# Performance work log

Hardware: AMD Instinct MI355X
Metric: run time of the kernel (lower is better)

Reference implementation:

```python
import jax, jax.numpy as jnp
import numpy as np

B, T, D, E, H, K = 4, 4096, 1024, 8, 512, 2  # batch, seq, n_embed, num_experts, bottleneck, top_k


def setup_inputs() -> dict:
    key = jax.random.key(0)
    ks = jax.random.split(key, 8)
    s = 0.02  # param scale (original zero-inits adapters; random used for a meaningful baseline)
    return {
        "x": jax.random.normal(ks[0], (B, T, D), jnp.float32),
        "Wr": (jax.random.normal(ks[1], (D, E), jnp.float32) * s),
        "br": jnp.zeros((E,), jnp.float32),
        "Wn": (jax.random.normal(ks[2], (D, E), jnp.float32) * s),
        "bn": jnp.zeros((E,), jnp.float32),
        "Wd": (jax.random.normal(ks[3], (E, D, H), jnp.float32) * s),
        "bd": jnp.zeros((E, H), jnp.float32),
        "Wu": (jax.random.normal(ks[4], (E, H, D), jnp.float32) * s),
        "bu": jnp.zeros((E, D), jnp.float32),
        "noise": jax.random.normal(ks[5], (B, T, E), jnp.float32),
        "top_k": K,
    }


def reference(x, Wr, br, Wn, bn, Wd, bd, Wu, bu, noise, top_k):
    # --- NoisyTopkRouter ---
    logits = x @ Wr + br                                   # [B,T,E]
    noise_logits = x @ Wn + bn                             # [B,T,E]
    noisy = logits + noise * jax.nn.softplus(noise_logits)  # randn * softplus(noise_logits)
    _, idx = jax.lax.top_k(noisy, top_k)                   # [B,T,K]
    # mask of selected experts; where(mask, noisy, -inf) == scatter(top_k_logits into -inf)
    mask = jax.nn.one_hot(idx, noisy.shape[-1], dtype=jnp.bool_).any(axis=-2)  # [B,T,E]
    sparse = jnp.where(mask, noisy, -jnp.inf)
    gates = jax.nn.softmax(sparse, axis=-1)                # zeros for unselected experts

    # --- Experts (dense grouped form; gate==0 exactly kills unselected experts incl. biases) ---
    down = jnp.einsum('btd,edh->bteh', x, Wd) + bd         # [B,T,E,H]
    hidden = jax.nn.gelu(down, approximate=False)          # torch GELU is exact (erf)
    up = jnp.einsum('bteh,ehd->bted', hidden, Wu) + bu     # [B,T,E,D]
    return jnp.einsum('bted,bte->btd', up, gates)          # gate-weighted combine
```

## Files before the change

kernel.cpp:

```cpp
#include <hip/hip_runtime.h>
#include <hip/hip_bf16.h>
#include <hip/hip_fp16.h>
#include <math.h>

#define DD   1024
#define EE   8
#define HH   512
#define NTOK 16384
#define NG   16
#define MAXMT 24

typedef __attribute__((ext_vector_type(8))) short short8;
typedef __attribute__((ext_vector_type(4))) float floatx4;

__device__ __forceinline__ ushort f2bfu(float f) {
    __hip_bfloat16 h = __float2bfloat16(f);
    return *reinterpret_cast<ushort*>(&h);
}
__device__ __forceinline__ float bfu2f(ushort u) {
    union { unsigned u; float f; } cv; cv.u = ((unsigned)u) << 16; return cv.f;
}

__device__ __forceinline__ void glds16(const void* g, void* l) {
    __builtin_amdgcn_global_load_lds(
        (const __attribute__((address_space(1))) unsigned int*)g,
        (__attribute__((address_space(3))) unsigned int*)l, 16, 0, 0);
}

__global__ __launch_bounds__(256) void trans_k(const float* __restrict__ src, ushort* __restrict__ dst,
                                               const int R, const int C, int* __restrict__ cnt) {
    if (cnt && blockIdx.x == 0 && blockIdx.y == 0 && blockIdx.z == 0 && threadIdx.x < 256)
        cnt[threadIdx.x] = 0;
    const int e = blockIdx.z, r0 = blockIdx.y * 64, c0 = blockIdx.x * 64;
    __shared__ float t[64][65];
    const int tid = threadIdx.x;
    const int cseg = (tid & 15) * 4, rr = tid >> 4;
#pragma unroll
    for (int j = 0; j < 4; ++j) {
        const int r = rr + j * 16;
        const float4 v = *(const float4*)(src + ((size_t)e * R + r0 + r) * C + c0 + cseg);
        t[r][cseg] = v.x; t[r][cseg+1] = v.y; t[r][cseg+2] = v.z; t[r][cseg+3] = v.w;
    }
    __syncthreads();
    const int rseg = (tid & 15) * 4;
#pragma unroll
    for (int j = 0; j < 4; ++j) {
        const int crow = (tid >> 4) + j * 16;
        ushort o[4];
#pragma unroll
        for (int q = 0; q < 4; ++q) o[q] = f2bfu(t[rseg + q][crow]);
        *(uint2*)(dst + ((size_t)e * C + c0 + crow) * R + r0 + rseg) = *(uint2*)o;
    }
}

#define ROUTER_TAIL(AR, AN, T) do {                                           \
    const int t_ = (T);                                                       \
    float noisy[EE];                                                          \
    _Pragma("unroll")                                                         \
    for (int e = 0; e < EE; ++e) {                                            \
        const float lg = AR[e] + br[e];                                       \
        const float nl = AN[e] + bn[e];                                       \
        const float sp = fmaxf(nl, 0.f) + log1pf(expf(-fabsf(nl)));           \
        noisy[e] = lg + noise[(size_t)t_ * EE + e] * sp;                      \
    }                                                                         \
    int i0 = 0;                                                               \
    _Pragma("unroll")                                                         \
    for (int e = 1; e < EE; ++e) if (noisy[e] > noisy[i0]) i0 = e;            \
    int i1 = (i0 == 0) ? 1 : 0;                                               \
    _Pragma("unroll")                                                         \
    for (int e = 0; e < EE; ++e) if (e != i0 && noisy[e] > noisy[i1]) i1 = e; \
    const float ex = expf(noisy[i1] - noisy[i0]);                             \
    const float g0 = 1.f / (1.f + ex);                                        \
    const float g1 = ex / (1.f + ex);                                         \
    __half h0 = __float2half_rn(g0), h1 = __float2half_rn(g1);                \
    const unsigned u0 = (unsigned)t_ | ((unsigned)*reinterpret_cast<ushort*>(&h0) << 16); \
    const unsigned u1 = (unsigned)t_ | ((unsigned)*reinterpret_cast<ushort*>(&h1) << 16); \
    const int ga = i0 * 2 + 0, gb = i1 * 2 + 1;                               \
    int p0 = atomicAdd(&cnt[ga * 16], 1);                                     \
    entries[ga * NTOK + p0] = u0;                                             \
    int p1 = atomicAdd(&cnt[gb * 16], 1);                                     \
    entries[gb * NTOK + p1] = u1;                                             \
} while (0)

__global__ __launch_bounds__(512) void router_k(
    const float* __restrict__ x, const float* __restrict__ Wr, const float* __restrict__ br,
    const float* __restrict__ Wn, const float* __restrict__ bn, const float* __restrict__ noise,
    int* __restrict__ cnt, unsigned* __restrict__ entries, ushort* __restrict__ xb)
{
    __shared__ __align__(16) float WT[DD * 20];

    const int tid = threadIdx.x;
    {
        const int d0 = tid * 2;
#pragma unroll
        for (int r = 0; r < 2; ++r) {
            const int d = d0 + r;
            float4 a = *(const float4*)(Wr + (size_t)d * EE);
            float4 b = *(const float4*)(Wr + (size_t)d * EE + 4);
            float4 c = *(const float4*)(Wn + (size_t)d * EE);
            float4 e4 = *(const float4*)(Wn + (size_t)d * EE + 4);
            float* row = &WT[d * 20];
            *(float4*)(row + 0)  = a;
            *(float4*)(row + 4)  = b;
            *(float4*)(row + 8)  = c;
            *(float4*)(row + 12) = e4;
        }
    }
    __syncthreads();

    const int wave = tid >> 6;
    const int lane = tid & 63;
    const int t0 = blockIdx.x * 16 + wave * 2;

    float a0r[EE], a0n[EE], a1r[EE], a1n[EE];
#pragma unroll
    for (int e = 0; e < EE; ++e) { a0r[e] = 0.f; a0n[e] = 0.f; a1r[e] = 0.f; a1n[e] = 0.f; }

    const float* xr0 = x + (size_t)t0 * DD;
    const float* xr1 = xr0 + DD;
    ushort* xb0 = xb + (size_t)t0 * DD;
    ushort* xb1 = xb0 + DD;

#pragma unroll 4
    for (int s = 0; s < DD / 64; ++s) {
        const int d = s * 64 + lane;
        const float x0 = xr0[d];
        const float x1 = xr1[d];
        xb0[d] = f2bfu(x0);
        xb1[d] = f2bfu(x1);
        const float* row = &WT[d * 20];
        const float4 w0 = *(const float4*)(row + 0);
        const float4 w1 = *(const float4*)(row + 4);
        const float4 w2 = *(const float4*)(row + 8);
        const float4 w3 = *(const float4*)(row + 12);
        const float wr[8] = { w0.x, w0.y, w0.z, w0.w, w1.x, w1.y, w1.z, w1.w };
        const float wn[8] = { w2.x, w2.y, w2.z, w2.w, w3.x, w3.y, w3.z, w3.w };
#pragma unroll
        for (int e = 0; e < EE; ++e) {
            a0r[e] = fmaf(x0, wr[e], a0r[e]);
            a0n[e] = fmaf(x0, wn[e], a0n[e]);
            a1r[e] = fmaf(x1, wr[e], a1r[e]);
            a1n[e] = fmaf(x1, wn[e], a1n[e]);
        }
    }
#pragma unroll
    for (int off = 32; off > 0; off >>= 1) {
#pragma unroll
        for (int e = 0; e < EE; ++e) {
            a0r[e] += __shfl_xor(a0r[e], off);
            a0n[e] += __shfl_xor(a0n[e], off);
            a1r[e] += __shfl_xor(a1r[e], off);
            a1n[e] += __shfl_xor(a1n[e], off);
        }
    }
    if (lane == 0) {
        ROUTER_TAIL(a0r, a0n, t0);
        ROUTER_TAIL(a1r, a1n, t0 + 1);
    }
}


__global__ __launch_bounds__(256) void down_k(
    const ushort* __restrict__ xb, const ushort* __restrict__ WdT, const float* __restrict__ bd,
    const int* __restrict__ cnt, const unsigned* __restrict__ entries, ushort* __restrict__ hid)
{
    const int bx = blockIdx.x;
    const int n0 = (bx & 3) * 128;
    const int tmg = bx >> 2;
    const int tm = tmg % MAXMT;
    const int g = tmg / MAXMT, e = g >> 1;
    const int n_g = cnt[g * 16];
    if (tm * 128 >= n_g) return;

    int og = 0;
    for (int gg = 0; gg < g; ++gg) og += cnt[gg * 16];

    __shared__ __align__(16) ushort As[128 * 64];
    __shared__ __align__(16) ushort Bs[128 * 64];
    __shared__ unsigned ecache[128];

    const int tid = threadIdx.x, lane = tid & 63, w = tid >> 6;
    const int wm = w >> 1, wn = w & 1;
    const int fr = lane & 15, fq = lane >> 4;

    if (tid < 128) {
        const int ridx = min(tm * 128 + tid, n_g - 1);
        ecache[tid] = entries[g * NTOK + ridx];
    }
    __syncthreads();

    const int lr = lane >> 3, seg = lane & 7;
    const int slog = seg ^ lr;
    const ushort* gA[4]; const ushort* gB[4];
    char* lA[4]; char* lB[4];
    const ushort* WTe = WdT + (size_t)e * HH * DD;
#pragma unroll
    for (int j = 0; j < 4; ++j) {
        const int row = w * 32 + j * 8 + lr;
        const int tok = (int)(ecache[row] & 0xFFFFu);
        gA[j] = xb + (size_t)tok * DD + slog * 8;
        gB[j] = WTe + (size_t)(n0 + row) * DD + slog * 8;
        lA[j] = (char*)As + (size_t)(w * 256 + j * 64) * 16;
        lB[j] = (char*)Bs + (size_t)(w * 256 + j * 64) * 16;
    }

    floatx4 acc[4][4];
#pragma unroll
    for (int i = 0; i < 4; ++i)
#pragma unroll
        for (int j = 0; j < 4; ++j) acc[i][j] = (floatx4){0.f, 0.f, 0.f, 0.f};

    const int axr = wm * 64 + fr;
    const int bxr = wn * 64 + fr;

    for (int k0 = 0; k0 < DD; k0 += 64) {
        __syncthreads();
#pragma unroll
        for (int j = 0; j < 4; ++j) { glds16(gA[j] + k0, lA[j]); glds16(gB[j] + k0, lB[j]); }
        __syncthreads();
#pragma unroll
        for (int kh = 0; kh < 2; ++kh) {
            short8 a[4], b[4];
#pragma unroll
            for (int mt = 0; mt < 4; ++mt) {
                const int r = axr + mt * 16;
                a[mt] = *(const short8*)&As[r * 64 + ((kh * 4 + fq) ^ (r & 7)) * 8];
            }
#pragma unroll
            for (int nt = 0; nt < 4; ++nt) {
                const int r = bxr + nt * 16;
                b[nt] = *(const short8*)&Bs[r * 64 + ((kh * 4 + fq) ^ (r & 7)) * 8];
            }
#pragma unroll
            for (int mt = 0; mt < 4; ++mt)
#pragma unroll
                for (int nt = 0; nt < 4; ++nt)
                    acc[mt][nt] = __builtin_amdgcn_mfma_f32_16x16x32_bf16(a[mt], b[nt], acc[mt][nt], 0, 0, 0);
        }
    }

    const int hbase = og + tm * 128;
#pragma unroll
    for (int nt = 0; nt < 4; ++nt) {
        const int n = n0 + wn * 64 + nt * 16 + fr;
        const float bias = bd[e * HH + n];
#pragma unroll
        for (int mt = 0; mt < 4; ++mt)
#pragma unroll
            for (int i = 0; i < 4; ++i) {
                const int rl = wm * 64 + mt * 16 + fq * 4 + i;
                if (tm * 128 + rl < n_g) {
                    const float v = acc[mt][nt][i] + bias;
                    const float ge = 0.5f * v * (1.f + erff(v * 0.7071067811865475f));
                    hid[(size_t)(hbase + rl) * HH + n] = f2bfu(ge);
                }
            }
    }
}

__global__ __launch_bounds__(256) void up_k(
    const ushort* __restrict__ hid, const ushort* __restrict__ WuT, const float* __restrict__ bu,
    const int* __restrict__ cnt, const unsigned* __restrict__ entries, ushort* __restrict__ slots)
{
    const int bx = blockIdx.x;
    const int n0 = (bx & 7) * 128;
    const int tmg = bx >> 3;
    const int tm = tmg % MAXMT;
    const int g = tmg / MAXMT, e = g >> 1, slot = g & 1;
    const int n_g = cnt[g * 16];
    if (tm * 128 >= n_g) return;

    int hbase = 0;
    for (int gg = 0; gg < g; ++gg) hbase += cnt[gg * 16];

    __shared__ __align__(16) ushort As[128 * 64];
    __shared__ __align__(16) ushort Bs[128 * 64];
    __shared__ unsigned ecache[128];

    const int tid = threadIdx.x, lane = tid & 63, w = tid >> 6;
    const int wm = w >> 1, wn = w & 1;
    const int fr = lane & 15, fq = lane >> 4;

    if (tid < 128) {
        const int ridx = min(tm * 128 + tid, n_g - 1);
        ecache[tid] = entries[g * NTOK + ridx];
    }
    __syncthreads();

    const int lr = lane >> 3, seg = lane & 7;
    const int slog = seg ^ lr;
    const ushort* gA[4]; const ushort* gB[4];
    char* lA[4]; char* lB[4];
    const ushort* WTe = WuT + (size_t)e * DD * HH;
#pragma unroll
    for (int j = 0; j < 4; ++j) {
        const int row = w * 32 + j * 8 + lr;
        const int ar = min(tm * 128 + row, n_g - 1);
        gA[j] = hid + (size_t)(hbase + ar) * HH + slog * 8;
        gB[j] = WTe + (size_t)(n0 + row) * HH + slog * 8;
        lA[j] = (char*)As + (size_t)(w * 256 + j * 64) * 16;
        lB[j] = (char*)Bs + (size_t)(w * 256 + j * 64) * 16;
    }

    floatx4 acc[4][4];
#pragma unroll
    for (int i = 0; i < 4; ++i)
#pragma unroll
        for (int j = 0; j < 4; ++j) acc[i][j] = (floatx4){0.f, 0.f, 0.f, 0.f};

    const int axr = wm * 64 + fr;
    const int bxr = wn * 64 + fr;

    for (int k0 = 0; k0 < HH; k0 += 64) {
        __syncthreads();
#pragma unroll
        for (int j = 0; j < 4; ++j) { glds16(gA[j] + k0, lA[j]); glds16(gB[j] + k0, lB[j]); }
        __syncthreads();
#pragma unroll
        for (int kh = 0; kh < 2; ++kh) {
            short8 a[4], b[4];
#pragma unroll
            for (int mt = 0; mt < 4; ++mt) {
                const int r = axr + mt * 16;
                a[mt] = *(const short8*)&As[r * 64 + ((kh * 4 + fq) ^ (r & 7)) * 8];
            }
#pragma unroll
            for (int nt = 0; nt < 4; ++nt) {
                const int r = bxr + nt * 16;
                b[nt] = *(const short8*)&Bs[r * 64 + ((kh * 4 + fq) ^ (r & 7)) * 8];
            }
#pragma unroll
            for (int mt = 0; mt < 4; ++mt)
#pragma unroll
                for (int nt = 0; nt < 4; ++nt)
                    acc[mt][nt] = __builtin_amdgcn_mfma_f32_16x16x32_bf16(a[mt], b[nt], acc[mt][nt], 0, 0, 0);
        }
    }

#pragma unroll
    for (int nt = 0; nt < 4; ++nt) {
        const int n = n0 + wn * 64 + nt * 16 + fr;
        const float bias = bu[e * DD + n];
#pragma unroll
        for (int mt = 0; mt < 4; ++mt)
#pragma unroll
            for (int i = 0; i < 4; ++i) {
                const int rl = wm * 64 + mt * 16 + fq * 4 + i;
                if (tm * 128 + rl < n_g) {
                    const unsigned en = ecache[rl];
                    const int tok = (int)(en & 0xFFFFu);
                    ushort hb = (ushort)(en >> 16);
                    const float gate = __half2float(*reinterpret_cast<__half*>(&hb));
                    const float v = (acc[mt][nt][i] + bias) * gate;
                    slots[((size_t)tok * 2 + slot) * DD + n] = f2bfu(v);
                }
            }
    }
}

__global__ __launch_bounds__(256) void combine_k(
    const ushort* __restrict__ slots, float* __restrict__ out)
{
    const size_t flat = ((size_t)blockIdx.x * 256 + threadIdx.x) * 8;
    const size_t t = flat >> 10;
    const size_t d = flat & (DD - 1);
    union { uint4 v; ushort h[8]; } a, b;
    a.v = *(const uint4*)(slots + ((t * 2 + 0) << 10) + d);
    b.v = *(const uint4*)(slots + ((t * 2 + 1) << 10) + d);
    float o[8];
#pragma unroll
    for (int j = 0; j < 8; ++j) o[j] = bfu2f(a.h[j]) + bfu2f(b.h[j]);
    *(float4*)(out + flat) = *(const float4*)&o[0];
    *(float4*)(out + flat + 4) = *(const float4*)&o[4];
}

extern "C" void kernel_launch(void* const* d_in, const int* in_sizes, int n_in,
                              void* d_out, int out_size, void* d_ws, size_t ws_size,
                              hipStream_t stream)
{
    const float* x     = (const float*)d_in[0];
    const float* Wr    = (const float*)d_in[1];
    const float* br    = (const float*)d_in[2];
    const float* Wn    = (const float*)d_in[3];
    const float* bn    = (const float*)d_in[4];
    const float* Wd    = (const float*)d_in[5];
    const float* bd    = (const float*)d_in[6];
    const float* Wu    = (const float*)d_in[7];
    const float* bu    = (const float*)d_in[8];
    const float* noise = (const float*)d_in[9];

    char* ws = (char*)d_ws;
    int*      cnt     = (int*)(ws + 0);
    unsigned* entries = (unsigned*)(ws + 2048);
    ushort*   xb      = (ushort*)(ws + 1050624);
    ushort*   WdT     = (ushort*)(ws + 34605056);
    ushort*   WuT     = (ushort*)(ws + 42993664);
    ushort*   hid     = (ushort*)(ws + 51382272);
    ushort*   slots   = (ushort*)(ws + 84936704);

    trans_k<<<dim3(HH / 64, DD / 64, EE), 256, 0, stream>>>(Wd, WdT, DD, HH, cnt);
    trans_k<<<dim3(DD / 64, HH / 64, EE), 256, 0, stream>>>(Wu, WuT, HH, DD, nullptr);
    router_k<<<NTOK / 16, 512, 0, stream>>>(x, Wr, br, Wn, bn, noise, cnt, entries, xb);
    down_k<<<NG * MAXMT * 4, 256, 0, stream>>>(xb, WdT, bd, cnt, entries, hid);
    up_k<<<NG * MAXMT * 8, 256, 0, stream>>>(hid, WuT, bu, cnt, entries, slots);
    combine_k<<<(NTOK * DD) / (256 * 8), 256, 0, stream>>>(slots, (float*)d_out);
}
```

Baseline: 427.5 us.

## Double-buffer LDS tiles in expert GEMMs and reorder block-to-tile mapping

Both expert GEMM kernels (down_k and up_k) now use two LDS buffers. The next K-slice is issued with global_load_lds while MFMAs run on the current slice, which leaves one barrier per iteration instead of two. This is meant to hide global-load latency behind compute. The block index decomposition is also changed so the N-tile is the slowest-varying index, which changes which blocks run together and share weight or activation tiles in cache. LDS use per block doubles, which may lower occupancy.

```diff
diff --git a/kernel.cpp b/kernel.cpp
--- a/kernel.cpp
+++ b/kernel.cpp
@@ -9,6 +9,7 @@
 #define NTOK 16384
 #define NG   16
 #define MAXMT 24
+#define NT   (NG * MAXMT)
 
 typedef __attribute__((ext_vector_type(8))) short short8;
 typedef __attribute__((ext_vector_type(4))) float floatx4;
@@ -165,8 +166,8 @@
     const int* __restrict__ cnt, const unsigned* __restrict__ entries, ushort* __restrict__ hid)
 {
     const int bx = blockIdx.x;
-    const int n0 = (bx & 3) * 128;
-    const int tmg = bx >> 2;
+    const int n0 = (bx / NT) * 128;
+    const int tmg = bx % NT;
     const int tm = tmg % MAXMT;
     const int g = tmg / MAXMT, e = g >> 1;
     const int n_g = cnt[g * 16];
@@ -175,8 +176,8 @@
     int og = 0;
     for (int gg = 0; gg < g; ++gg) og += cnt[gg * 16];
 
-    __shared__ __align__(16) ushort As[128 * 64];
-    __shared__ __align__(16) ushort Bs[128 * 64];
+    __shared__ __align__(16) ushort As[2 * 128 * 64];
+    __shared__ __align__(16) ushort Bs[2 * 128 * 64];
     __shared__ unsigned ecache[128];
 
     const int tid = threadIdx.x, lane = tid & 63, w = tid >> 6;
@@ -192,7 +193,7 @@
     const int lr = lane >> 3, seg = lane & 7;
     const int slog = seg ^ lr;
     const ushort* gA[4]; const ushort* gB[4];
-    char* lA[4]; char* lB[4];
+    int loff[4];
     const ushort* WTe = WdT + (size_t)e * HH * DD;
 #pragma unroll
     for (int j = 0; j < 4; ++j) {
@@ -200,8 +201,7 @@
         const int tok = (int)(ecache[row] & 0xFFFFu);
         gA[j] = xb + (size_t)tok * DD + slog * 8;
         gB[j] = WTe + (size_t)(n0 + row) * DD + slog * 8;
-        lA[j] = (char*)As + (size_t)(w * 256 + j * 64) * 16;
-        lB[j] = (char*)Bs + (size_t)(w * 256 + j * 64) * 16;
+        loff[j] = (w * 256 + j * 64) * 16;
     }
 
     floatx4 acc[4][4];
@@ -213,23 +213,36 @@
     const int axr = wm * 64 + fr;
     const int bxr = wn * 64 + fr;
 
+#pragma unroll
+    for (int j = 0; j < 4; ++j) {
+        glds16(gA[j], (char*)As + loff[j]);
+        glds16(gB[j], (char*)Bs + loff[j]);
+    }
+    __syncthreads();
+
+    int cur = 0;
     for (int k0 = 0; k0 < DD; k0 += 64) {
-        __syncthreads();
-#pragma unroll
-        for (int j = 0; j < 4; ++j) { glds16(gA[j] + k0, lA[j]); glds16(gB[j] + k0, lB[j]); }
-        __syncthreads();
+        if (k0 + 64 < DD) {
+            const int nb = (cur ^ 1) * 16384;
+#pragma unroll
+            for (int j = 0; j < 4; ++j) {
+                glds16(gA[j] + k0 + 64, (char*)As + nb + loff[j]);
+                glds16(gB[j] + k0 + 64, (char*)Bs + nb + loff[j]);
+            }
+        }
+        const int cb = cur * 8192;
 #pragma unroll
         for (int kh = 0; kh < 2; ++kh) {
             short8 a[4], b[4];
 #pragma unroll
             for (int mt = 0; mt < 4; ++mt) {
                 const int r = axr + mt * 16;
-                a[mt] = *(const short8*)&As[r * 64 + ((kh * 4 + fq) ^ (r & 7)) * 8];
+                a[mt] = *(const short8*)&As[cb + r * 64 + ((kh * 4 + fq) ^ (r & 7)) * 8];
             }
 #pragma unroll
             for (int nt = 0; nt < 4; ++nt) {
                 const int r = bxr + nt * 16;
-                b[nt] = *(const short8*)&Bs[r * 64 + ((kh * 4 + fq) ^ (r & 7)) * 8];
+                b[nt] = *(const short8*)&Bs[cb + r * 64 + ((kh * 4 + fq) ^ (r & 7)) * 8];
             }
 #pragma unroll
             for (int mt = 0; mt < 4; ++mt)
@@ -237,6 +250,8 @@
                 for (int nt = 0; nt < 4; ++nt)
                     acc[mt][nt] = __builtin_amdgcn_mfma_f32_16x16x32_bf16(a[mt], b[nt], acc[mt][nt], 0, 0, 0);
         }
+        __syncthreads();
+        cur ^= 1;
     }
 
     const int hbase = og + tm * 128;
@@ -263,8 +278,8 @@
     const int* __restrict__ cnt, const unsigned* __restrict__ entries, ushort* __restrict__ slots)
 {
     const int bx = blockIdx.x;
-    const int n0 = (bx & 7) * 128;
-    const int tmg = bx >> 3;
+    const int n0 = (bx / NT) * 128;
+    const int tmg = bx % NT;
     const int tm = tmg % MAXMT;
     const int g = tmg / MAXMT, e = g >> 1, slot = g & 1;
     const int n_g = cnt[g * 16];
@@ -273,8 +288,8 @@
     int hbase = 0;
     for (int gg = 0; gg < g; ++gg) hbase += cnt[gg * 16];
 
-    __shared__ __align__(16) ushort As[128 * 64];
-    __shared__ __align__(16) ushort Bs[128 * 64];
+    __shared__ __align__(16) ushort As[2 * 128 * 64];
+    __shared__ __align__(16) ushort Bs[2 * 128 * 64];
     __shared__ unsigned ecache[128];
 
     const int tid = threadIdx.x, lane = tid & 63, w = tid >> 6;
@@ -290,7 +305,7 @@
     const int lr = lane >> 3, seg = lane & 7;
     const int slog = seg ^ lr;
     const ushort* gA[4]; const ushort* gB[4];
-    char* lA[4]; char* lB[4];
+    int loff[4];
     const ushort* WTe = WuT + (size_t)e * DD * HH;
 #pragma unroll
     for (int j = 0; j < 4; ++j) {
@@ -298,8 +313,7 @@
         const int ar = min(tm * 128 + row, n_g - 1);
         gA[j] = hid + (size_t)(hbase + ar) * HH + slog * 8;
         gB[j] = WTe + (size_t)(n0 + row) * HH + slog * 8;
-        lA[j] = (char*)As + (size_t)(w * 256 + j * 64) * 16;
-        lB[j] = (char*)Bs + (size_t)(w * 256 + j * 64) * 16;
+        loff[j] = (w * 256 + j * 64) * 16;
     }
 
     floatx4 acc[4][4];
@@ -311,23 +325,36 @@
     const int axr = wm * 64 + fr;
     const int bxr = wn * 64 + fr;
 
+#pragma unroll
+    for (int j = 0; j < 4; ++j) {
+        glds16(gA[j], (char*)As + loff[j]);
+        glds16(gB[j], (char*)Bs + loff[j]);
+    }
+    __syncthreads();
+
+    int cur = 0;
     for (int k0 = 0; k0 < HH; k0 += 64) {
-        __syncthreads();
-#pragma unroll
-        for (int j = 0; j < 4; ++j) { glds16(gA[j] + k0, lA[j]); glds16(gB[j] + k0, lB[j]); }
-        __syncthreads();
+        if (k0 + 64 < HH) {
+            const int nb = (cur ^ 1) * 16384;
+#pragma unroll
+            for (int j = 0; j < 4; ++j) {
+                glds16(gA[j] + k0 + 64, (char*)As + nb + loff[j]);
+                glds16(gB[j] + k0 + 64, (char*)Bs + nb + loff[j]);
+            }
+        }
+        const int cb = cur * 8192;
 #pragma unroll
         for (int kh = 0; kh < 2; ++kh) {
             short8 a[4], b[4];
 #pragma unroll
             for (int mt = 0; mt < 4; ++mt) {
                 const int r = axr + mt * 16;
-                a[mt] = *(const short8*)&As[r * 64 + ((kh * 4 + fq) ^ (r & 7)) * 8];
+                a[mt] = *(const short8*)&As[cb + r * 64 + ((kh * 4 + fq) ^ (r & 7)) * 8];
             }
 #pragma unroll
             for (int nt = 0; nt < 4; ++nt) {
                 const int r = bxr + nt * 16;
-                b[nt] = *(const short8*)&Bs[r * 64 + ((kh * 4 + fq) ^ (r & 7)) * 8];
+                b[nt] = *(const short8*)&Bs[cb + r * 64 + ((kh * 4 + fq) ^ (r & 7)) * 8];
             }
 #pragma unroll
             for (int mt = 0; mt < 4; ++mt)
@@ -335,6 +362,8 @@
                 for (int nt = 0; nt < 4; ++nt)
                     acc[mt][nt] = __builtin_amdgcn_mfma_f32_16x16x32_bf16(a[mt], b[nt], acc[mt][nt], 0, 0, 0);
         }
+        __syncthreads();
+        cur ^= 1;
     }
 
 #pragma unroll
@@ -401,7 +430,7 @@
     trans_k<<<dim3(HH / 64, DD / 64, EE), 256, 0, stream>>>(Wd, WdT, DD, HH, cnt);
     trans_k<<<dim3(DD / 64, HH / 64, EE), 256, 0, stream>>>(Wu, WuT, HH, DD, nullptr);
     router_k<<<NTOK / 16, 512, 0, stream>>>(x, Wr, br, Wn, bn, noise, cnt, entries, xb);
-    down_k<<<NG * MAXMT * 4, 256, 0, stream>>>(xb, WdT, bd, cnt, entries, hid);
-    up_k<<<NG * MAXMT * 8, 256, 0, stream>>>(hid, WuT, bu, cnt, entries, slots);
+    down_k<<<NT * 4, 256, 0, stream>>>(xb, WdT, bd, cnt, entries, hid);
+    up_k<<<NT * 8, 256, 0, stream>>>(hid, WuT, bu, cnt, entries, slots);
     combine_k<<<(NTOK * DD) / (256 * 8), 256, 0, stream>>>(slots, (float*)d_out);
 }
```

New measurement: 456.0 us. +6.7%, slower.
